# Optimization experiments

Hardware: AMD Instinct MI355X
Metric: run time of the kernel (lower is better)

## Reference

```python
import jax, jax.numpy as jnp
import numpy as np

N_NODES = 50000
N_EDGES = 800000
IN_CH = 64
HID = 128
OUT_AGE, OUT_SEX, OUT_ETH = 21, 2, 5


def _glorot(key, shape):
    fan_in, fan_out = shape
    lim = float(np.sqrt(6.0 / (fan_in + fan_out)))
    return jax.random.uniform(key, shape, jnp.float32, -lim, lim)


def sage_conv(x, src, dst, Wl, Wr, b, n_nodes):
    # PyG SAGEConv (mean aggr): out = lin_l(mean_{j->i} x_j) + lin_r(x_i) + bias
    msg_sum = jax.ops.segment_sum(x[src], dst, num_segments=n_nodes)  # [N, d]
    deg = jax.ops.segment_sum(jnp.ones((src.shape[0],), x.dtype), dst,
                              num_segments=n_nodes)  # [N]
    mean = msg_sum / jnp.maximum(deg, 1.0)[:, None]
    return mean @ Wl + x @ Wr + b


def setup_inputs() -> dict:
    key = jax.random.key(0)
    ks = jax.random.split(key, 16)
    x = jax.random.normal(ks[0], (N_NODES, IN_CH), jnp.float32)
    edge_src = jax.random.randint(ks[1], (N_EDGES,), 0, N_NODES)
    edge_dst = jax.random.randint(ks[2], (N_EDGES,), 0, N_NODES)
    dims = [(IN_CH, HID), (HID, HID), (HID, HID),
            (HID, OUT_AGE), (HID, OUT_SEX), (HID, OUT_ETH)]
    names = ['1', '2', '3', 'age', 'sex', 'eth']
    inp = {'x': x, 'edge_src': edge_src, 'edge_dst': edge_dst}
    for i, (nm, (di, do)) in enumerate(zip(names, dims)):
        inp[f'Wl_{nm}'] = _glorot(ks[3 + 2 * i], (di, do))
        inp[f'Wr_{nm}'] = _glorot(ks[4 + 2 * i], (di, do))
        inp[f'b_{nm}'] = jnp.zeros((do,), jnp.float32)
    return inp


def reference(x, edge_src, edge_dst,
              Wl_1, Wr_1, b_1, Wl_2, Wr_2, b_2, Wl_3, Wr_3, b_3,
              Wl_age, Wr_age, b_age, Wl_sex, Wr_sex, b_sex,
              Wl_eth, Wr_eth, b_eth):
    n = x.shape[0]
    h = jax.nn.relu(sage_conv(x, edge_src, edge_dst, Wl_1, Wr_1, b_1, n))
    h = jax.nn.relu(sage_conv(h, edge_src, edge_dst, Wl_2, Wr_2, b_2, n))
    h = jax.nn.relu(sage_conv(h, edge_src, edge_dst, Wl_3, Wr_3, b_3, n))
    age = sage_conv(h, edge_src, edge_dst, Wl_age, Wr_age, b_age, n)
    sex = sage_conv(h, edge_src, edge_dst, Wl_sex, Wr_sex, b_sex, n)
    eth = sage_conv(h, edge_src, edge_dst, Wl_eth, Wr_eth, b_eth, n)
    return (age, sex, eth)
```

## Files before the change

kernel.cpp:

```cpp
#include <hip/hip_runtime.h>
#include <hip/hip_bf16.h>


typedef __attribute__((ext_vector_type(8))) short bf16x8;
typedef __attribute__((ext_vector_type(4))) float f32x4;

#define NBSH 7
#define EPW  4096

__device__ __forceinline__ unsigned short f2b(float f) {
    __hip_bfloat16 h = __float2bfloat16(f);
    return *reinterpret_cast<unsigned short*>(&h);
}
__device__ __forceinline__ float b2f(unsigned short u) {
    __hip_bfloat16 h;
    *reinterpret_cast<unsigned short*>(&h) = u;
    return __bfloat162float(h);
}

__global__ void bucket_hist(const int* __restrict__ dst, int* __restrict__ ghist,
                            int n_edges, int nb) {
    __shared__ int lh[512];
    int tid = threadIdx.x;
    for (int i = tid; i < 512; i += 256) lh[i] = 0;
    __syncthreads();
    int stride = gridDim.x * blockDim.x;
    for (int e = blockIdx.x * blockDim.x + tid; e < n_edges; e += stride)
        atomicAdd(&lh[dst[e] >> NBSH], 1);
    __syncthreads();
    for (int i = tid; i < nb; i += 256)
        if (lh[i]) atomicAdd(&ghist[i], lh[i]);
}

__global__ void scan_buckets(const int* __restrict__ hist, int* __restrict__ base,
                             int* __restrict__ cur, int nb, int n_edges) {
    __shared__ int tmp[512];
    int t = threadIdx.x;
    int v = (t < nb) ? hist[t] : 0;
    tmp[t] = v;
    __syncthreads();
    for (int off = 1; off < 512; off <<= 1) {
        int u = (t >= off) ? tmp[t - off] : 0;
        __syncthreads();
        tmp[t] += u;
        __syncthreads();
    }
    if (t < nb) {
        base[t] = tmp[t] - v;
        cur[t] = tmp[t] - v;
    }
    if (t == 0) base[nb] = n_edges;
}

__global__ __launch_bounds__(512) void bin_edges_lds(
    const int* __restrict__ src, const int* __restrict__ dst,
    int* __restrict__ bkt_cur, uint2* __restrict__ ebuf, int n_edges, int nb) {
    __shared__ int hist[512];
    __shared__ int hbase[513];
    __shared__ int hcur[512];
    __shared__ uint2 sorted[EPW];
    int tid = threadIdx.x;
    int chunk0 = blockIdx.x * EPW;
    int cnt = min(EPW, n_edges - chunk0);
    hist[tid] = 0;
    __syncthreads();
    for (int i = tid; i < cnt; i += 512) atomicAdd(&hist[dst[chunk0 + i] >> NBSH], 1);
    __syncthreads();
    int v = hist[tid];
    hbase[tid] = v;
    __syncthreads();
    for (int off = 1; off < 512; off <<= 1) {
        int u = (tid >= off) ? hbase[tid - off] : 0;
        __syncthreads();
        hbase[tid] += u;
        __syncthreads();
    }
    int excl = hbase[tid] - v;
    __syncthreads();
    hbase[tid] = excl;
    hcur[tid] = excl;
    if (tid == 511) hbase[512] = excl + v;
    __syncthreads();
    for (int i = tid; i < cnt; i += 512) {
        int s = src[chunk0 + i];
        int d = dst[chunk0 + i];
        int p = atomicAdd(&hcur[d >> NBSH], 1);
        sorted[p] = make_uint2((unsigned)s, (unsigned)d);
    }
    __syncthreads();
    int cntb = hbase[tid + 1] - hbase[tid];
    int gb = 0;
    if (tid < nb && cntb > 0) gb = atomicAdd(&bkt_cur[tid], cntb);
    hist[tid] = gb;
    __syncthreads();
    for (int i = tid; i < cnt; i += 512) {
        uint2 ed = sorted[i];
        int b = (int)(ed.y >> NBSH);
        ebuf[hist[b] + (i - hbase[b])] = ed;
    }
}

__global__ void bucket_degi(const uint2* __restrict__ ebuf, const int* __restrict__ bkt_base,
                            int* __restrict__ degi, int n_nodes) {
    __shared__ int ld[128];
    int b = blockIdx.x, tid = threadIdx.x;
    int lo = b << NBSH;
    if (tid < 128) ld[tid] = 0;
    __syncthreads();
    int s = bkt_base[b], t = bkt_base[b + 1];
    for (int i = s + tid; i < t; i += 256) atomicAdd(&ld[(int)ebuf[i].y - lo], 1);
    __syncthreads();
    int hi = min(lo + 128, n_nodes);
    if (tid < hi - lo) degi[lo + tid] = ld[tid];
}

__global__ void scan_local(const int* __restrict__ degi, int* __restrict__ loc,
                           int* __restrict__ bsum, int n) {
    __shared__ int tmp[256];
    int i = blockIdx.x * 256 + threadIdx.x;
    int v = (i < n) ? degi[i] : 0;
    tmp[threadIdx.x] = v;
    __syncthreads();
    for (int off = 1; off < 256; off <<= 1) {
        int t = (threadIdx.x >= off) ? tmp[threadIdx.x - off] : 0;
        __syncthreads();
        tmp[threadIdx.x] += t;
        __syncthreads();
    }
    if (i < n) loc[i] = tmp[threadIdx.x] - v;
    if (threadIdx.x == 255) bsum[blockIdx.x] = tmp[255];
}

__global__ void scan_block(int* __restrict__ bsum, int nblk) {
    __shared__ int tmp[256];
    int v = (threadIdx.x < nblk) ? bsum[threadIdx.x] : 0;
    tmp[threadIdx.x] = v;
    __syncthreads();
    for (int off = 1; off < 256; off <<= 1) {
        int t = (threadIdx.x >= off) ? tmp[threadIdx.x - off] : 0;
        __syncthreads();
        tmp[threadIdx.x] += t;
        __syncthreads();
    }
    if (threadIdx.x < nblk) bsum[threadIdx.x] = tmp[threadIdx.x] - v;
}

__global__ void scan_add(const int* __restrict__ loc, const int* __restrict__ bsum,
                         int* __restrict__ row_start, int n, int n_edges) {
    int i = blockIdx.x * 256 + threadIdx.x;
    if (i < n) row_start[i] = loc[i] + bsum[blockIdx.x];
    if (i == 0) row_start[n] = n_edges;
}

__global__ void scatter2(const uint2* __restrict__ ebuf, const int* __restrict__ bkt_base,
                         const int* __restrict__ row_start, int* __restrict__ col,
                         int n_nodes) {
    __shared__ int lcur[128];
    int b = blockIdx.x, tid = threadIdx.x;
    int lo = b << NBSH;
    int hi = min(lo + 128, n_nodes);
    if (tid < hi - lo) lcur[tid] = row_start[lo + tid];
    __syncthreads();
    int s = bkt_base[b], t = bkt_base[b + 1];
    for (int i = s + tid; i < t; i += 256) {
        uint2 ed = ebuf[i];
        int p = atomicAdd(&lcur[(int)ed.y - lo], 1);
        col[p] = (int)ed.x;
    }
}

__device__ __forceinline__ void bt_body(const float* __restrict__ Wl,
                                        const float* __restrict__ Wr,
                                        unsigned short* __restrict__ Bt,
                                        int KA, int idx) {
    int KTOT = 2 * KA;
    if (idx >= 128 * KTOT) return;
    int n = idx / KTOT, k = idx % KTOT;
    float v = (k < KA) ? Wl[k * 128 + n] : Wr[(k - KA) * 128 + n];
    Bt[idx] = f2b(v);
}

__global__ void prep_all(const float* __restrict__ x, unsigned short* __restrict__ xb, int n4,
                         const float* __restrict__ Wl1, const float* __restrict__ Wr1,
                         unsigned short* __restrict__ Bt1,
                         const float* __restrict__ Wl2, const float* __restrict__ Wr2,
                         unsigned short* __restrict__ Bt2,
                         const float* __restrict__ Wl3, const float* __restrict__ Wr3,
                         unsigned short* __restrict__ Bt3,
                         const float* __restrict__ Wl_age, const float* __restrict__ Wl_sex,
                         const float* __restrict__ Wl_eth,
                         const float* __restrict__ Wr_age, const float* __restrict__ Wr_sex,
                         const float* __restrict__ Wr_eth,
                         const float* __restrict__ b_age, const float* __restrict__ b_sex,
                         const float* __restrict__ b_eth,
                         float* __restrict__ Wl_cat, float* __restrict__ Wr_cat,
                         float* __restrict__ b_cat) {
    int nbx = (n4 + 255) / 256;
    int b = blockIdx.x;
    if (b < nbx) {
        int t = b * 256 + threadIdx.x;
        if (t < n4) {
            float4 v = reinterpret_cast<const float4*>(x)[t];
            uint2 o;
            o.x = (unsigned)f2b(v.x) | ((unsigned)f2b(v.y) << 16);
            o.y = (unsigned)f2b(v.z) | ((unsigned)f2b(v.w) << 16);
            reinterpret_cast<uint2*>(xb)[t] = o;
        }
        return;
    }
    b -= nbx;
    if (b < 64)  { bt_body(Wl1, Wr1, Bt1, 64,  b * 256 + threadIdx.x); return; }
    b -= 64;
    if (b < 128) { bt_body(Wl2, Wr2, Bt2, 128, b * 256 + threadIdx.x); return; }
    b -= 128;
    if (b < 128) { bt_body(Wl3, Wr3, Bt3, 128, b * 256 + threadIdx.x); return; }
    b -= 128;
    {
        int idx = b * 256 + threadIdx.x;
        if (idx < 128 * 28) {
            int k = idx / 28, j = idx % 28;
            float vl, vr;
            if (j < 21) {
                vl = Wl_age[k * 21 + j];
                vr = Wr_age[k * 21 + j];
            } else if (j < 23) {
                vl = Wl_sex[k * 2 + (j - 21)];
                vr = Wr_sex[k * 2 + (j - 21)];
            } else {
                vl = Wl_eth[k * 5 + (j - 23)];
                vr = Wr_eth[k * 5 + (j - 23)];
            }
            Wl_cat[idx] = vl;
            Wr_cat[idx] = vr;
        }
        if (idx < 28)
            b_cat[idx] = (idx < 21) ? b_age[idx] : (idx < 23) ? b_sex[idx - 21] : b_eth[idx - 23];
    }
}

__global__ void agg128_bf(const unsigned short* __restrict__ feat,
                          const int* __restrict__ row_start, const int* __restrict__ col,
                          unsigned short* __restrict__ mean, int n_nodes) {
    int wave = (blockIdx.x * blockDim.x + threadIdx.x) >> 6;
    int lane = threadIdx.x & 63;
    if (wave >= n_nodes) return;
    int s0 = row_start[wave];
    int deg = row_start[wave + 1] - s0;
    const unsigned* f2 = reinterpret_cast<const unsigned*>(feat);
    float a0 = 0.f, a1 = 0.f, b0 = 0.f, b1 = 0.f;
    float c0 = 0.f, c1 = 0.f, d0 = 0.f, d1 = 0.f;
    for (int base = 0; base < deg; base += 64) {
        int blk = min(64, deg - base);
        int cv = col[s0 + base + min(lane, blk - 1)];
        int i = 0;
        for (; i + 3 < blk; i += 4) {
            int e0 = __shfl(cv, i), e1 = __shfl(cv, i + 1);
            int e2 = __shfl(cv, i + 2), e3 = __shfl(cv, i + 3);
            unsigned u0 = f2[(size_t)e0 * 64 + lane];
            unsigned u1 = f2[(size_t)e1 * 64 + lane];
            unsigned u2 = f2[(size_t)e2 * 64 + lane];
            unsigned u3 = f2[(size_t)e3 * 64 + lane];
            a0 += b2f((unsigned short)(u0 & 0xffff)); a1 += b2f((unsigned short)(u0 >> 16));
            b0 += b2f((unsigned short)(u1 & 0xffff)); b1 += b2f((unsigned short)(u1 >> 16));
            c0 += b2f((unsigned short)(u2 & 0xffff)); c1 += b2f((unsigned short)(u2 >> 16));
            d0 += b2f((unsigned short)(u3 & 0xffff)); d1 += b2f((unsigned short)(u3 >> 16));
        }
        for (; i < blk; ++i) {
            int e0 = __shfl(cv, i);
            unsigned u0 = f2[(size_t)e0 * 64 + lane];
            a0 += b2f((unsigned short)(u0 & 0xffff)); a1 += b2f((unsigned short)(u0 >> 16));
        }
    }
    float inv = (deg > 0) ? 1.0f / (float)deg : 0.0f;
    float sA = (a0 + b0) + (c0 + d0);
    float sB = (a1 + b1) + (c1 + d1);
    unsigned o = (unsigned)f2b(sA * inv) | ((unsigned)f2b(sB * inv) << 16);
    reinterpret_cast<unsigned*>(mean)[(size_t)wave * 64 + lane] = o;
}

__global__ void agg64_bf(const unsigned short* __restrict__ feat,
                         const int* __restrict__ row_start, const int* __restrict__ col,
                         unsigned short* __restrict__ mean, int n_nodes) {
    int wave = (blockIdx.x * blockDim.x + threadIdx.x) >> 6;
    int lane = threadIdx.x & 63;
    if (wave >= n_nodes) return;
    int half = lane >> 5;
    int lp = lane & 31;
    int s0 = row_start[wave];
    int deg = row_start[wave + 1] - s0;
    const unsigned* f2 = reinterpret_cast<const unsigned*>(feat);
    float a0 = 0.f, a1 = 0.f, b0 = 0.f, b1 = 0.f;
    float c0 = 0.f, c1 = 0.f, d0 = 0.f, d1 = 0.f;
    for (int base = 0; base < deg; base += 64) {
        int blk = min(64, deg - base);
        int cv = col[s0 + base + min(lane, blk - 1)];
        int nfull = blk & ~7;
        for (int i = half * 4; i < nfull; i += 8) {
            int e0 = __shfl(cv, i), e1 = __shfl(cv, i + 1);
            int e2 = __shfl(cv, i + 2), e3 = __shfl(cv, i + 3);
            unsigned u0 = f2[(size_t)e0 * 32 + lp];
            unsigned u1 = f2[(size_t)e1 * 32 + lp];
            unsigned u2 = f2[(size_t)e2 * 32 + lp];
            unsigned u3 = f2[(size_t)e3 * 32 + lp];
            a0 += b2f((unsigned short)(u0 & 0xffff)); a1 += b2f((unsigned short)(u0 >> 16));
            b0 += b2f((unsigned short)(u1 & 0xffff)); b1 += b2f((unsigned short)(u1 >> 16));
            c0 += b2f((unsigned short)(u2 & 0xffff)); c1 += b2f((unsigned short)(u2 >> 16));
            d0 += b2f((unsigned short)(u3 & 0xffff)); d1 += b2f((unsigned short)(u3 >> 16));
        }
        int tstart = nfull + half * 4;
        int tend = min(blk, tstart + 4);
        for (int i = tstart; i < tend; ++i) {
            int e0 = __shfl(cv, i);
            unsigned u0 = f2[(size_t)e0 * 32 + lp];
            a0 += b2f((unsigned short)(u0 & 0xffff)); a1 += b2f((unsigned short)(u0 >> 16));
        }
    }
    float sA = (a0 + b0) + (c0 + d0);
    float sB = (a1 + b1) + (c1 + d1);
    sA += __shfl_down(sA, 32);
    sB += __shfl_down(sB, 32);
    if (half == 0) {
        float inv = (deg > 0) ? 1.0f / (float)deg : 0.0f;
        unsigned o = (unsigned)f2b(sA * inv) | ((unsigned)f2b(sB * inv) << 16);
        reinterpret_cast<unsigned*>(mean)[(size_t)wave * 32 + lp] = o;
    }
}

template <int KTOT, int KA>
__global__ __launch_bounds__(256) void mfma_layer(
    const unsigned short* __restrict__ A0, const unsigned short* __restrict__ A1,
    const unsigned short* __restrict__ Bt, const float* __restrict__ bias,
    unsigned short* __restrict__ out, int n_nodes) {
    constexpr int KC = KTOT / 64;
    __shared__ __align__(16) unsigned short sA[64][72];
    __shared__ __align__(16) unsigned short sB[128][72];
    int node0 = blockIdx.x * 64;
    int tid = threadIdx.x;
    int w = tid >> 6, lane = tid & 63;
    f32x4 acc[8] = {};
    for (int kc = 0; kc < KC; ++kc) {
        const unsigned short* Asrc;
        int kbase, aw;
        if (kc * 64 < KA) { Asrc = A0; kbase = kc * 64; aw = KA; }
        else              { Asrc = A1; kbase = kc * 64 - KA; aw = KTOT - KA; }
        {
            int nd = tid >> 2, k16 = (tid & 3) * 16;
            uint4 v0 = {0, 0, 0, 0}, v1 = {0, 0, 0, 0};
            int gn = node0 + nd;
            if (gn < n_nodes) {
                const uint4* src = reinterpret_cast<const uint4*>(Asrc + (size_t)gn * aw + kbase + k16);
                v0 = src[0];
                v1 = src[1];
            }
            uint4* dst = reinterpret_cast<uint4*>(&sA[nd][k16]);
            dst[0] = v0;
            dst[1] = v1;
        }
        {
            int n = tid >> 1, k32 = (tid & 1) * 32;
            const uint4* src = reinterpret_cast<const uint4*>(Bt + (size_t)n * KTOT + kc * 64 + k32);
            uint4* dst = reinterpret_cast<uint4*>(&sB[n][k32]);
            dst[0] = src[0];
            dst[1] = src[1];
            dst[2] = src[2];
            dst[3] = src[3];
        }
        __syncthreads();
#pragma unroll
        for (int ks = 0; ks < 2; ++ks) {
            int kl = ks * 32 + (lane >> 4) * 8;
            bf16x8 af = *reinterpret_cast<const bf16x8*>(&sA[w * 16 + (lane & 15)][kl]);
#pragma unroll
            for (int t = 0; t < 8; ++t) {
                bf16x8 bfr = *reinterpret_cast<const bf16x8*>(&sB[t * 16 + (lane & 15)][kl]);
                acc[t] = __builtin_amdgcn_mfma_f32_16x16x32_bf16(af, bfr, acc[t], 0, 0, 0);
            }
        }
        __syncthreads();
    }
    int r0 = w * 16, cq = lane >> 4, cr = lane & 15;
#pragma unroll
    for (int t = 0; t < 8; ++t) {
        int colj = t * 16 + cr;
        float bv = bias[colj];
#pragma unroll
        for (int i = 0; i < 4; ++i) {
            int node = node0 + r0 + cq * 4 + i;
            if (node < n_nodes) {
                float v = fmaxf(acc[t][i] + bv, 0.0f);
                out[(size_t)node * 128 + colj] = f2b(v);
            }
        }
    }
}

__global__ void proj_kernel(const unsigned short* __restrict__ h,
                            const float* __restrict__ Wl_cat, float* __restrict__ p,
                            int n_nodes) {
    const int NPB = 4;
    int node0 = blockIdx.x * NPB;
    __shared__ float sh[NPB][128];
    for (int idx = threadIdx.x; idx < NPB * 128; idx += blockDim.x) {
        int n = idx >> 7, k = idx & 127;
        int node = node0 + n;
        if (node < n_nodes) sh[n][k] = b2f(h[(size_t)node * 128 + k]);
    }
    __syncthreads();
    int n = threadIdx.x >> 5, j = threadIdx.x & 31;
    int node = node0 + n;
    if (node >= n_nodes) return;
    float acc = 0.f;
    if (j < 28)
        for (int k = 0; k < 128; k++) acc += sh[n][k] * Wl_cat[k * 28 + j];
    p[(size_t)node * 32 + j] = acc;
}

__global__ void agg_gather32(const float* __restrict__ p, const int* __restrict__ row_start,
                             const int* __restrict__ col, float* __restrict__ meanp,
                             int n_nodes) {
    int node = (blockIdx.x * blockDim.x + threadIdx.x) >> 5;
    int lane = threadIdx.x & 63;
    int lp = lane & 31;
    int grpbase = lane & 32;
    if (node >= n_nodes) return;
    int s0 = row_start[node];
    int deg = row_start[node + 1] - s0;
    float a = 0.f, b = 0.f, c = 0.f, d = 0.f;
    for (int base = 0; base < deg; base += 32) {
        int blk = min(32, deg - base);
        int cv = col[s0 + base + min(lp, blk - 1)];
        int i = 0;
        for (; i + 3 < blk; i += 4) {
            int e0 = __shfl(cv, grpbase + i),     e1 = __shfl(cv, grpbase + i + 1);
            int e2 = __shfl(cv, grpbase + i + 2), e3 = __shfl(cv, grpbase + i + 3);
            a += p[(size_t)e0 * 32 + lp];
            b += p[(size_t)e1 * 32 + lp];
            c += p[(size_t)e2 * 32 + lp];
            d += p[(size_t)e3 * 32 + lp];
        }
        for (; i < blk; ++i) {
            int e0 = __shfl(cv, grpbase + i);
            a += p[(size_t)e0 * 32 + lp];
        }
    }
    float inv = (deg > 0) ? 1.0f / (float)deg : 0.0f;
    meanp[(size_t)node * 32 + lp] = ((a + b) + (c + d)) * inv;
}

__global__ void head_out_kernel(const unsigned short* __restrict__ h,
                                const float* __restrict__ meanp,
                                const float* __restrict__ Wr_cat, const float* __restrict__ b_cat,
                                float* __restrict__ age, float* __restrict__ sex,
                                float* __restrict__ eth, int n_nodes) {
    const int NPB = 4;
    int node0 = blockIdx.x * NPB;
    __shared__ float sh[NPB][128];
    for (int idx = threadIdx.x; idx < NPB * 128; idx += blockDim.x) {
        int n = idx >> 7, k = idx & 127;
        int node = node0 + n;
        if (node < n_nodes) sh[n][k] = b2f(h[(size_t)node * 128 + k]);
    }
    __syncthreads();
    int n = threadIdx.x >> 5, j = threadIdx.x & 31;
    int node = node0 + n;
    if (node >= n_nodes || j >= 28) return;
    float acc = b_cat[j] + meanp[(size_t)node * 32 + j];
    for (int k = 0; k < 128; k++) acc += sh[n][k] * Wr_cat[k * 28 + j];
    if (j < 21)
        age[(size_t)node * 21 + j] = acc;
    else if (j < 23)
        sex[(size_t)node * 2 + (j - 21)] = acc;
    else
        eth[(size_t)node * 5 + (j - 23)] = acc;
}

extern "C" void kernel_launch(void* const* d_in, const int* in_sizes, int n_in,
                              void* d_out, int out_size, void* d_ws, size_t ws_size,
                              hipStream_t stream) {
    const float* x        = (const float*)d_in[0];
    const int*   edge_src = (const int*)d_in[1];
    const int*   edge_dst = (const int*)d_in[2];
    const float* Wl_1 = (const float*)d_in[3];
    const float* Wr_1 = (const float*)d_in[4];
    const float* b_1  = (const float*)d_in[5];
    const float* Wl_2 = (const float*)d_in[6];
    const float* Wr_2 = (const float*)d_in[7];
    const float* b_2  = (const float*)d_in[8];
    const float* Wl_3 = (const float*)d_in[9];
    const float* Wr_3 = (const float*)d_in[10];
    const float* b_3  = (const float*)d_in[11];
    const float* Wl_age = (const float*)d_in[12];
    const float* Wr_age = (const float*)d_in[13];
    const float* b_age  = (const float*)d_in[14];
    const float* Wl_sex = (const float*)d_in[15];
    const float* Wr_sex = (const float*)d_in[16];
    const float* b_sex  = (const float*)d_in[17];
    const float* Wl_eth = (const float*)d_in[18];
    const float* Wr_eth = (const float*)d_in[19];
    const float* b_eth  = (const float*)d_in[20];

    const int n_nodes = in_sizes[0] / 64;
    const int n_edges = in_sizes[1];

    char* ws = (char*)d_ws;
    int*            degi      = (int*)(ws + 0);
    int*            row_start = (int*)(ws + 200192);
    int*            col       = (int*)(ws + 600576);
    unsigned short* Bt1       = (unsigned short*)(ws + 3800832);
    unsigned short* Bt2       = (unsigned short*)(ws + 3833600);
    unsigned short* Bt3       = (unsigned short*)(ws + 3899136);
    float*          Wl_cat    = (float*)(ws + 3964672);
    float*          Wr_cat    = (float*)(ws + 3979008);
    float*          b_cat     = (float*)(ws + 3993344);
    unsigned short* xb        = (unsigned short*)(ws + 3993600);
    unsigned short* h_bf      = (unsigned short*)(ws + 10393856);
    unsigned short* mean_bf   = (unsigned short*)(ws + 23194112);
    float*          p         = (float*)(ws + 35994368);
    float*          meanp     = (float*)(ws + 42394624);
    int*            scan_loc  = (int*)(ws + 48794880);
    int*            scan_bsum = (int*)(ws + 48995072);
    uint2*          ebuf      = (uint2*)p;
    int*            bkt_hist  = (int*)meanp;
    int*            bkt_base  = bkt_hist + 512;
    int*            bkt_cur   = bkt_hist + 1032;

    float* out_age = (float*)d_out;
    float* out_sex = out_age + (size_t)n_nodes * 21;
    float* out_eth = out_sex + (size_t)n_nodes * 2;

    const int nb        = (n_nodes + 127) >> NBSH;
    const int nchunks   = (n_edges + EPW - 1) / EPW;
    const int nblk_scan = (n_nodes + 255) / 256;
    const int n4        = n_nodes * 64 / 4;

    hipMemsetAsync(bkt_hist, 0, 512 * sizeof(int), stream);
    bucket_hist<<<256, 256, 0, stream>>>(edge_dst, bkt_hist, n_edges, nb);
    scan_buckets<<<1, 512, 0, stream>>>(bkt_hist, bkt_base, bkt_cur, nb, n_edges);
    bin_edges_lds<<<nchunks, 512, 0, stream>>>(edge_src, edge_dst, bkt_cur, ebuf, n_edges, nb);
    bucket_degi<<<nb, 256, 0, stream>>>(ebuf, bkt_base, degi, n_nodes);
    scan_local<<<nblk_scan, 256, 0, stream>>>(degi, scan_loc, scan_bsum, n_nodes);
    scan_block<<<1, 256, 0, stream>>>(scan_bsum, nblk_scan);
    scan_add<<<nblk_scan, 256, 0, stream>>>(scan_loc, scan_bsum, row_start, n_nodes, n_edges);
    scatter2<<<nb, 256, 0, stream>>>(ebuf, bkt_base, row_start, col, n_nodes);

    {
        int grid = (n4 + 255) / 256 + 64 + 128 + 128 + 14;
        prep_all<<<grid, 256, 0, stream>>>(
            x, xb, n4, Wl_1, Wr_1, Bt1, Wl_2, Wr_2, Bt2, Wl_3, Wr_3, Bt3,
            Wl_age, Wl_sex, Wl_eth, Wr_age, Wr_sex, Wr_eth, b_age, b_sex, b_eth,
            Wl_cat, Wr_cat, b_cat);
    }

    const int agg_grid  = (n_nodes * 64 + 255) / 256;
    const int gemm_grid = (n_nodes + 63) / 64;

    agg64_bf<<<agg_grid, 256, 0, stream>>>(xb, row_start, col, mean_bf, n_nodes);
    mfma_layer<128, 64><<<gemm_grid, 256, 0, stream>>>(mean_bf, xb, Bt1, b_1, h_bf, n_nodes);

    agg128_bf<<<agg_grid, 256, 0, stream>>>(h_bf, row_start, col, mean_bf, n_nodes);
    mfma_layer<256, 128><<<gemm_grid, 256, 0, stream>>>(mean_bf, h_bf, Bt2, b_2, h_bf, n_nodes);

    agg128_bf<<<agg_grid, 256, 0, stream>>>(h_bf, row_start, col, mean_bf, n_nodes);
    mfma_layer<256, 128><<<gemm_grid, 256, 0, stream>>>(mean_bf, h_bf, Bt3, b_3, h_bf, n_nodes);

    proj_kernel<<<(n_nodes + 3) / 4, 128, 0, stream>>>(h_bf, Wl_cat, p, n_nodes);
    agg_gather32<<<(n_nodes * 32 + 255) / 256, 256, 0, stream>>>(p, row_start, col, meanp, n_nodes);
    head_out_kernel<<<(n_nodes + 3) / 4, 128, 0, stream>>>(
        h_bf, meanp, Wr_cat, b_cat, out_age, out_sex, out_eth, n_nodes);
}
```

Before: 348.5 us.

## Fuse CSR degree/scan/scatter into per-bucket sort and merge head kernels

Replaces the degree-count, three-pass global scan and scatter kernels with one per-bucket kernel. It builds a local histogram, scans it in LDS, writes row_start from the bucket base, and scatters col in place. This works because the buckets are already contiguous in destination order. The head path now computes both the Wl and Wr projections in one kernel, and the neighbour gather adds the root term and writes the outputs directly, which removes the meanp round trip and one launch. The bucket histogram zeroing moves into prep_all, so the memset call goes away and prep_all runs first.

```diff
diff --git a/kernel.cpp b/kernel.cpp
--- a/kernel.cpp
+++ b/kernel.cpp
@@ -100,72 +100,39 @@
     }
 }
 
-__global__ void bucket_degi(const uint2* __restrict__ ebuf, const int* __restrict__ bkt_base,
-                            int* __restrict__ degi, int n_nodes) {
-    __shared__ int ld[128];
+__global__ void sort_bucket(const uint2* __restrict__ ebuf, const int* __restrict__ bkt_base,
+                            int* __restrict__ row_start, int* __restrict__ col,
+                            int n_nodes, int n_edges) {
+    __shared__ int hist[128];
+    __shared__ int sc[128];
+    __shared__ int hcur[128];
     int b = blockIdx.x, tid = threadIdx.x;
     int lo = b << NBSH;
-    if (tid < 128) ld[tid] = 0;
+    if (tid < 128) hist[tid] = 0;
     __syncthreads();
     int s = bkt_base[b], t = bkt_base[b + 1];
-    for (int i = s + tid; i < t; i += 256) atomicAdd(&ld[(int)ebuf[i].y - lo], 1);
-    __syncthreads();
-    int hi = min(lo + 128, n_nodes);
-    if (tid < hi - lo) degi[lo + tid] = ld[tid];
-}
-
-__global__ void scan_local(const int* __restrict__ degi, int* __restrict__ loc,
-                           int* __restrict__ bsum, int n) {
-    __shared__ int tmp[256];
-    int i = blockIdx.x * 256 + threadIdx.x;
-    int v = (i < n) ? degi[i] : 0;
-    tmp[threadIdx.x] = v;
-    __syncthreads();
-    for (int off = 1; off < 256; off <<= 1) {
-        int t = (threadIdx.x >= off) ? tmp[threadIdx.x - off] : 0;
-        __syncthreads();
-        tmp[threadIdx.x] += t;
-        __syncthreads();
-    }
-    if (i < n) loc[i] = tmp[threadIdx.x] - v;
-    if (threadIdx.x == 255) bsum[blockIdx.x] = tmp[255];
-}
-
-__global__ void scan_block(int* __restrict__ bsum, int nblk) {
-    __shared__ int tmp[256];
-    int v = (threadIdx.x < nblk) ? bsum[threadIdx.x] : 0;
-    tmp[threadIdx.x] = v;
-    __syncthreads();
-    for (int off = 1; off < 256; off <<= 1) {
-        int t = (threadIdx.x >= off) ? tmp[threadIdx.x - off] : 0;
-        __syncthreads();
-        tmp[threadIdx.x] += t;
-        __syncthreads();
-    }
-    if (threadIdx.x < nblk) bsum[threadIdx.x] = tmp[threadIdx.x] - v;
-}
-
-__global__ void scan_add(const int* __restrict__ loc, const int* __restrict__ bsum,
-                         int* __restrict__ row_start, int n, int n_edges) {
-    int i = blockIdx.x * 256 + threadIdx.x;
-    if (i < n) row_start[i] = loc[i] + bsum[blockIdx.x];
-    if (i == 0) row_start[n] = n_edges;
-}
-
-__global__ void scatter2(const uint2* __restrict__ ebuf, const int* __restrict__ bkt_base,
-                         const int* __restrict__ row_start, int* __restrict__ col,
-                         int n_nodes) {
-    __shared__ int lcur[128];
-    int b = blockIdx.x, tid = threadIdx.x;
-    int lo = b << NBSH;
-    int hi = min(lo + 128, n_nodes);
-    if (tid < hi - lo) lcur[tid] = row_start[lo + tid];
-    __syncthreads();
-    int s = bkt_base[b], t = bkt_base[b + 1];
+    for (int i = s + tid; i < t; i += 256) atomicAdd(&hist[(int)ebuf[i].y - lo], 1);
+    __syncthreads();
+    if (tid < 128) sc[tid] = hist[tid];
+    __syncthreads();
+    for (int off = 1; off < 128; off <<= 1) {
+        int u = (tid < 128 && tid >= off) ? sc[tid - off] : 0;
+        __syncthreads();
+        if (tid < 128) sc[tid] += u;
+        __syncthreads();
+    }
+    if (tid < 128) {
+        int excl = sc[tid] - hist[tid];
+        hcur[tid] = excl;
+        int node = lo + tid;
+        if (node < n_nodes) row_start[node] = s + excl;
+    }
+    if (b == 0 && tid == 0) row_start[n_nodes] = n_edges;
+    __syncthreads();
     for (int i = s + tid; i < t; i += 256) {
         uint2 ed = ebuf[i];
-        int p = atomicAdd(&lcur[(int)ed.y - lo], 1);
-        col[p] = (int)ed.x;
+        int p = atomicAdd(&hcur[(int)ed.y - lo], 1);
+        col[s + p] = (int)ed.x;
     }
 }
 
@@ -194,7 +161,7 @@
                          const float* __restrict__ b_age, const float* __restrict__ b_sex,
                          const float* __restrict__ b_eth,
                          float* __restrict__ Wl_cat, float* __restrict__ Wr_cat,
-                         float* __restrict__ b_cat) {
+                         float* __restrict__ b_cat, int* __restrict__ bkt_hist) {
     int nbx = (n4 + 255) / 256;
     int b = blockIdx.x;
     if (b < nbx) {
@@ -215,7 +182,7 @@
     b -= 128;
     if (b < 128) { bt_body(Wl3, Wr3, Bt3, 128, b * 256 + threadIdx.x); return; }
     b -= 128;
-    {
+    if (b < 14) {
         int idx = b * 256 + threadIdx.x;
         if (idx < 128 * 28) {
             int k = idx / 28, j = idx % 28;
@@ -235,7 +202,10 @@
         }
         if (idx < 28)
             b_cat[idx] = (idx < 21) ? b_age[idx] : (idx < 23) ? b_sex[idx - 21] : b_eth[idx - 23];
-    }
+        return;
+    }
+    bkt_hist[threadIdx.x] = 0;
+    bkt_hist[256 + threadIdx.x] = 0;
 }
 
 __global__ void agg128_bf(const unsigned short* __restrict__ feat,
@@ -394,9 +364,10 @@
     }
 }
 
-__global__ void proj_kernel(const unsigned short* __restrict__ h,
-                            const float* __restrict__ Wl_cat, float* __restrict__ p,
-                            int n_nodes) {
+__global__ void proj2_kernel(const unsigned short* __restrict__ h,
+                             const float* __restrict__ Wl_cat, const float* __restrict__ Wr_cat,
+                             const float* __restrict__ b_cat,
+                             float* __restrict__ p, float* __restrict__ q, int n_nodes) {
     const int NPB = 4;
     int node0 = blockIdx.x * NPB;
     __shared__ float sh[NPB][128];
@@ -409,15 +380,24 @@
     int n = threadIdx.x >> 5, j = threadIdx.x & 31;
     int node = node0 + n;
     if (node >= n_nodes) return;
-    float acc = 0.f;
-    if (j < 28)
-        for (int k = 0; k < 128; k++) acc += sh[n][k] * Wl_cat[k * 28 + j];
-    p[(size_t)node * 32 + j] = acc;
-}
-
-__global__ void agg_gather32(const float* __restrict__ p, const int* __restrict__ row_start,
-                             const int* __restrict__ col, float* __restrict__ meanp,
-                             int n_nodes) {
+    float accp = 0.f;
+    float accq = 0.f;
+    if (j < 28) {
+        accq = b_cat[j];
+        for (int k = 0; k < 128; k++) {
+            float hv = sh[n][k];
+            accp += hv * Wl_cat[k * 28 + j];
+            accq += hv * Wr_cat[k * 28 + j];
+        }
+    }
+    p[(size_t)node * 32 + j] = accp;
+    q[(size_t)node * 32 + j] = accq;
+}
+
+__global__ void head_final(const float* __restrict__ p, const float* __restrict__ q,
+                           const int* __restrict__ row_start, const int* __restrict__ col,
+                           float* __restrict__ age, float* __restrict__ sex,
+                           float* __restrict__ eth, int n_nodes) {
     int node = (blockIdx.x * blockDim.x + threadIdx.x) >> 5;
     int lane = threadIdx.x & 63;
     int lp = lane & 31;
@@ -444,34 +424,13 @@
         }
     }
     float inv = (deg > 0) ? 1.0f / (float)deg : 0.0f;
-    meanp[(size_t)node * 32 + lp] = ((a + b) + (c + d)) * inv;
-}
-
-__global__ void head_out_kernel(const unsigned short* __restrict__ h,
-                                const float* __restrict__ meanp,
-                                const float* __restrict__ Wr_cat, const float* __restrict__ b_cat,
-                                float* __restrict__ age, float* __restrict__ sex,
-                                float* __restrict__ eth, int n_nodes) {
-    const int NPB = 4;
-    int node0 = blockIdx.x * NPB;
-    __shared__ float sh[NPB][128];
-    for (int idx = threadIdx.x; idx < NPB * 128; idx += blockDim.x) {
-        int n = idx >> 7, k = idx & 127;
-        int node = node0 + n;
-        if (node < n_nodes) sh[n][k] = b2f(h[(size_t)node * 128 + k]);
-    }
-    __syncthreads();
-    int n = threadIdx.x >> 5, j = threadIdx.x & 31;
-    int node = node0 + n;
-    if (node >= n_nodes || j >= 28) return;
-    float acc = b_cat[j] + meanp[(size_t)node * 32 + j];
-    for (int k = 0; k < 128; k++) acc += sh[n][k] * Wr_cat[k * 28 + j];
-    if (j < 21)
-        age[(size_t)node * 21 + j] = acc;
-    else if (j < 23)
-        sex[(size_t)node * 2 + (j - 21)] = acc;
-    else
-        eth[(size_t)node * 5 + (j - 23)] = acc;
+    float out = ((a + b) + (c + d)) * inv + q[(size_t)node * 32 + lp];
+    if (lp < 21)
+        age[(size_t)node * 21 + lp] = out;
+    else if (lp < 23)
+        sex[(size_t)node * 2 + (lp - 21)] = out;
+    else if (lp < 28)
+        eth[(size_t)node * 5 + (lp - 23)] = out;
 }
 
 extern "C" void kernel_launch(void* const* d_in, const int* in_sizes, int n_in,
@@ -503,7 +462,6 @@
     const int n_edges = in_sizes[1];
 
     char* ws = (char*)d_ws;
-    int*            degi      = (int*)(ws + 0);
     int*            row_start = (int*)(ws + 200192);
     int*            col       = (int*)(ws + 600576);
     unsigned short* Bt1       = (unsigned short*)(ws + 3800832);
@@ -516,11 +474,9 @@
     unsigned short* h_bf      = (unsigned short*)(ws + 10393856);
     unsigned short* mean_bf   = (unsigned short*)(ws + 23194112);
     float*          p         = (float*)(ws + 35994368);
-    float*          meanp     = (float*)(ws + 42394624);
-    int*            scan_loc  = (int*)(ws + 48794880);
-    int*            scan_bsum = (int*)(ws + 48995072);
+    float*          q         = (float*)(ws + 42394624);
     uint2*          ebuf      = (uint2*)p;
-    int*            bkt_hist  = (int*)meanp;
+    int*            bkt_hist  = (int*)q;
     int*            bkt_base  = bkt_hist + 512;
     int*            bkt_cur   = bkt_hist + 1032;
 
@@ -528,28 +484,22 @@
     float* out_sex = out_age + (size_t)n_nodes * 21;
     float* out_eth = out_sex + (size_t)n_nodes * 2;
 
-    const int nb        = (n_nodes + 127) >> NBSH;
-    const int nchunks   = (n_edges + EPW - 1) / EPW;
-    const int nblk_scan = (n_nodes + 255) / 256;
-    const int n4        = n_nodes * 64 / 4;
-
-    hipMemsetAsync(bkt_hist, 0, 512 * sizeof(int), stream);
+    const int nb      = (n_nodes + 127) >> NBSH;
+    const int nchunks = (n_edges + EPW - 1) / EPW;
+    const int n4      = n_nodes * 64 / 4;
+
+    {
+        int grid = (n4 + 255) / 256 + 64 + 128 + 128 + 14 + 1;
+        prep_all<<<grid, 256, 0, stream>>>(
+            x, xb, n4, Wl_1, Wr_1, Bt1, Wl_2, Wr_2, Bt2, Wl_3, Wr_3, Bt3,
+            Wl_age, Wl_sex, Wl_eth, Wr_age, Wr_sex, Wr_eth, b_age, b_sex, b_eth,
+            Wl_cat, Wr_cat, b_cat, bkt_hist);
+    }
+
     bucket_hist<<<256, 256, 0, stream>>>(edge_dst, bkt_hist, n_edges, nb);
     scan_buckets<<<1, 512, 0, stream>>>(bkt_hist, bkt_base, bkt_cur, nb, n_edges);
     bin_edges_lds<<<nchunks, 512, 0, stream>>>(edge_src, edge_dst, bkt_cur, ebuf, n_edges, nb);
-    bucket_degi<<<nb, 256, 0, stream>>>(ebuf, bkt_base, degi, n_nodes);
-    scan_local<<<nblk_scan, 256, 0, stream>>>(degi, scan_loc, scan_bsum, n_nodes);
-    scan_block<<<1, 256, 0, stream>>>(scan_bsum, nblk_scan);
-    scan_add<<<nblk_scan, 256, 0, stream>>>(scan_loc, scan_bsum, row_start, n_nodes, n_edges);
-    scatter2<<<nb, 256, 0, stream>>>(ebuf, bkt_base, row_start, col, n_nodes);
-
-    {
-        int grid = (n4 + 255) / 256 + 64 + 128 + 128 + 14;
-        prep_all<<<grid, 256, 0, stream>>>(
-            x, xb, n4, Wl_1, Wr_1, Bt1, Wl_2, Wr_2, Bt2, Wl_3, Wr_3, Bt3,
-            Wl_age, Wl_sex, Wl_eth, Wr_age, Wr_sex, Wr_eth, b_age, b_sex, b_eth,
-            Wl_cat, Wr_cat, b_cat);
-    }
+    sort_bucket<<<nb, 256, 0, stream>>>(ebuf, bkt_base, row_start, col, n_nodes, n_edges);
 
     const int agg_grid  = (n_nodes * 64 + 255) / 256;
     const int gemm_grid = (n_nodes + 63) / 64;
@@ -563,8 +513,7 @@
     agg128_bf<<<agg_grid, 256, 0, stream>>>(h_bf, row_start, col, mean_bf, n_nodes);
     mfma_layer<256, 128><<<gemm_grid, 256, 0, stream>>>(mean_bf, h_bf, Bt3, b_3, h_bf, n_nodes);
 
-    proj_kernel<<<(n_nodes + 3) / 4, 128, 0, stream>>>(h_bf, Wl_cat, p, n_nodes);
-    agg_gather32<<<(n_nodes * 32 + 255) / 256, 256, 0, stream>>>(p, row_start, col, meanp, n_nodes);
-    head_out_kernel<<<(n_nodes + 3) / 4, 128, 0, stream>>>(
-        h_bf, meanp, Wr_cat, b_cat, out_age, out_sex, out_eth, n_nodes);
-}
+    proj2_kernel<<<(n_nodes + 3) / 4, 128, 0, stream>>>(h_bf, Wl_cat, Wr_cat, b_cat, p, q, n_nodes);
+    head_final<<<(n_nodes * 32 + 255) / 256, 256, 0, stream>>>(
+        p, q, row_start, col, out_age, out_sex, out_eth, n_nodes);
+}
```

New measurement: 330.4 us. 5.2% less time.
